# Kernel optimization log

Hardware: AMD Instinct MI355X
Metric: run time of the kernel (lower is better)

Reference implementation:

```python
import jax, jax.numpy as jnp
import numpy as np

B, T, C, H = 8, 1024, 128, 8
BLOCK = 1024  # block_size; wpe has BLOCK+1 rows, last is padding (zeros)
E = C // H


def layer_norm(x, g, b, eps=1e-5):
    mu = jnp.mean(x, axis=-1, keepdims=True)
    var = jnp.var(x, axis=-1, keepdims=True)
    return (x - mu) * jax.lax.rsqrt(var + eps) * g + b


def setup_inputs() -> dict:
    key = jax.random.key(0)
    ks = jax.random.split(key, 7)
    x = jax.random.normal(ks[0], (B, T, C), dtype=jnp.float32)
    Wq = jax.random.normal(ks[1], (C, C), dtype=jnp.float32) * 0.02
    Wk = jax.random.normal(ks[2], (C, C), dtype=jnp.float32) * 0.02
    Wv = jax.random.normal(ks[3], (C, C), dtype=jnp.float32) * 0.02
    Wp = jax.random.normal(ks[4], (C, C), dtype=jnp.float32) * 0.02
    wpe = jax.random.normal(ks[5], (BLOCK + 1, C), dtype=jnp.float32) * 0.02
    wpe = wpe.at[BLOCK].set(0.0)  # padding_idx row is zero
    ln_g = jnp.ones((C,), dtype=jnp.float32)
    ln_b = jnp.zeros((C,), dtype=jnp.float32)
    return {"x": x, "Wq": Wq, "Wk": Wk, "Wv": Wv, "Wp": Wp,
            "wpe": wpe, "ln_g": ln_g, "ln_b": ln_b}


def reference(x, Wq, Wk, Wv, Wp, wpe, ln_g, ln_b):
    Bx, Tx, Cx = x.shape
    ln_x = layer_norm(x, ln_g, ln_b)
    # project and split heads: [B, H, T, E]
    q = (ln_x @ Wq).reshape(Bx, Tx, H, E).transpose(0, 2, 1, 3)
    k = (ln_x @ Wk).reshape(Bx, Tx, H, E).transpose(0, 2, 1, 3)
    v = (ln_x @ Wv).reshape(Bx, Tx, H, E).transpose(0, 2, 1, 3)
    # relative position indices: i-j, negatives -> padding row BLOCK
    i = jnp.arange(Tx)[:, None]
    j = jnp.arange(Tx)[None, :]
    rel_idx = jnp.where(i - j < 0, BLOCK, i - j)  # [T, T]
    rel = wpe[rel_idx].reshape(Tx, Tx, H, E)      # [T, T, H, E]
    scale = 1.0 / np.sqrt(E).astype(np.float32)
    scores = (jnp.einsum('bhte,bhse->bhts', q, k)
              + jnp.einsum('tshe,bhte->bhts', rel, q)) * scale
    causal = (j <= i)  # [T, T]
    scores = jnp.where(causal[None, None, :, :], scores, jnp.float32(-jnp.inf))
    attn = jax.nn.softmax(scores, axis=-1)
    y = jnp.einsum('bhts,bhse->bhte', attn, v)    # [B, H, T, E]
    y = y.transpose(0, 2, 1, 3).reshape(Bx, Tx, Cx)
    return y @ Wp + x
```

## Files before the change

### kernel.cpp

```cpp
#include <hip/hip_runtime.h>
#include <hip/hip_bf16.h>

#define B 8
#define T 1024
#define C 128
#define H 8
#define E 16
#define BH (B*H)
#define VSTR 17

typedef __attribute__((ext_vector_type(4)))  short bf16x4;
typedef __attribute__((ext_vector_type(8)))  short bf16x8;
typedef __attribute__((ext_vector_type(16))) float f32x16;
typedef __attribute__((ext_vector_type(2)))  int   int2v;

#define QSCALE 0.36067376022224085f

__device__ __forceinline__ unsigned short bfbits(float x) {
    __hip_bfloat16 h = __float2bfloat16(x);
    return __builtin_bit_cast(unsigned short, h);
}
__device__ __forceinline__ unsigned pack2(float a, float b) {
    return (unsigned)bfbits(a) | ((unsigned)bfbits(b) << 16);
}
__device__ __forceinline__ unsigned packtr(float a, float b) {
    return (__builtin_bit_cast(unsigned, a) >> 16) | (__builtin_bit_cast(unsigned, b) & 0xffff0000u);
}

__global__ __launch_bounds__(C) void k_prep(
    const float* __restrict__ wpe,
    const float* __restrict__ Wq, const float* __restrict__ Wk,
    const float* __restrict__ Wv, const float* __restrict__ Wp,
    __hip_bfloat16* __restrict__ Wpb,
    __hip_bfloat16* __restrict__ WT,
    __hip_bfloat16* __restrict__ WpT,
    ushort* __restrict__ VT)
{
    int bid = blockIdx.x, tid = threadIdx.x;
    if (bid < 1025) {
        int h = tid >> 4, e = tid & 15;
        Wpb[((size_t)h * 1025 + bid) * 16 + e] = __float2bfloat16(wpe[(size_t)bid * C + tid]);
    } else if (bid < 1537) {
        int n = bid - 1025;
        if (n < 128)      WT[n * C + tid]          = __float2bfloat16(Wq[tid * C + n] * QSCALE);
        else if (n < 256) WT[n * C + tid]          = __float2bfloat16(Wk[tid * C + (n - 128)]);
        else if (n < 384) WT[n * C + tid]          = __float2bfloat16(Wv[tid * C + (n - 256)]);
        else              WpT[(n - 384) * C + tid] = __float2bfloat16(Wp[tid * C + (n - 384)]);
    } else {
        int bh = bid - 1537;
        ushort* row = VT + ((size_t)bh * VSTR + 16) * T + tid * 8;
        uint2 ones = make_uint2(0x3F803F80u, 0x3F803F80u);
        *(uint2*)(row)     = ones;
        *(uint2*)(row + 4) = ones;
    }
}

__global__ __launch_bounds__(256) void k_qkv(
    const float* __restrict__ x, const float* __restrict__ g, const float* __restrict__ bb,
    const __hip_bfloat16* __restrict__ WT,
    __hip_bfloat16* __restrict__ Qb, __hip_bfloat16* __restrict__ Kb,
    __hip_bfloat16* __restrict__ VT)
{
    __shared__ ushort lnlds[32 * 132];
    const int tid = threadIdx.x;
    const int mt = blockIdx.x & 255, part = blockIdx.x >> 8;

    {
        const int r = tid >> 3, qq = tid & 7;
        const float* xp = x + ((size_t)mt * 32 + r) * C + qq * 16;
        float4 x0 = ((const float4*)xp)[0];
        float4 x1 = ((const float4*)xp)[1];
        float4 x2 = ((const float4*)xp)[2];
        float4 x3 = ((const float4*)xp)[3];
        float s1v = x0.x + x0.y + x0.z + x0.w + x1.x + x1.y + x1.z + x1.w
                  + x2.x + x2.y + x2.z + x2.w + x3.x + x3.y + x3.z + x3.w;
        float s2v = x0.x*x0.x + x0.y*x0.y + x0.z*x0.z + x0.w*x0.w
                  + x1.x*x1.x + x1.y*x1.y + x1.z*x1.z + x1.w*x1.w
                  + x2.x*x2.x + x2.y*x2.y + x2.z*x2.z + x2.w*x2.w
                  + x3.x*x3.x + x3.y*x3.y + x3.z*x3.z + x3.w*x3.w;
        s1v += __shfl_xor(s1v, 1, 64); s2v += __shfl_xor(s2v, 1, 64);
        s1v += __shfl_xor(s1v, 2, 64); s2v += __shfl_xor(s2v, 2, 64);
        s1v += __shfl_xor(s1v, 4, 64); s2v += __shfl_xor(s2v, 4, 64);
        float mu  = s1v * (1.f / C);
        float var = s2v * (1.f / C) - mu * mu;
        float rs  = rsqrtf(var + 1e-5f);
        const float4* gp = (const float4*)(g  + qq * 16);
        const float4* bp = (const float4*)(bb + qq * 16);
        float4 g0 = gp[0], g1 = gp[1], g2 = gp[2], g3 = gp[3];
        float4 b0 = bp[0], b1 = bp[1], b2 = bp[2], b3 = bp[3];
        #define LNV(xx, gg, bv) (((xx) - mu) * rs * (gg) + (bv))
        uint2* dst = (uint2*)&lnlds[r * 132 + qq * 16];
        dst[0] = make_uint2(pack2(LNV(x0.x,g0.x,b0.x), LNV(x0.y,g0.y,b0.y)),
                            pack2(LNV(x0.z,g0.z,b0.z), LNV(x0.w,g0.w,b0.w)));
        dst[1] = make_uint2(pack2(LNV(x1.x,g1.x,b1.x), LNV(x1.y,g1.y,b1.y)),
                            pack2(LNV(x1.z,g1.z,b1.z), LNV(x1.w,g1.w,b1.w)));
        dst[2] = make_uint2(pack2(LNV(x2.x,g2.x,b2.x), LNV(x2.y,g2.y,b2.y)),
                            pack2(LNV(x2.z,g2.z,b2.z), LNV(x2.w,g2.w,b2.w)));
        dst[3] = make_uint2(pack2(LNV(x3.x,g3.x,b3.x), LNV(x3.y,g3.y,b3.y)),
                            pack2(LNV(x3.z,g3.z,b3.z), LNV(x3.w,g3.w,b3.w)));
        #undef LNV
    }
    __syncthreads();

    const int wv = tid >> 6, lane = tid & 63, c = lane & 31, h5 = lane >> 5;
    const int b = mt >> 5, trow = (mt & 31) * 32;
    const int nt = part * 4 + wv, n0 = nt * 32;

    bf16x8 wf[8], lf[8];
    #pragma unroll
    for (int s = 0; s < 8; ++s)
        wf[s] = *(const bf16x8*)(WT + (size_t)(n0 + c) * C + 16 * s + 8 * h5);
    #pragma unroll
    for (int s = 0; s < 8; ++s) {
        const ushort* lp = &lnlds[c * 132 + 16 * s + 8 * h5];
        bf16x4 lo = *(const bf16x4*)lp;
        bf16x4 hi = *(const bf16x4*)(lp + 4);
        lf[s] = __builtin_shufflevector(lo, hi, 0, 1, 2, 3, 4, 5, 6, 7);
    }
    f32x16 acc;
    #pragma unroll
    for (int r = 0; r < 16; ++r) acc[r] = 0.f;

    if (nt < 8) {
        #pragma unroll
        for (int s = 0; s < 8; ++s)
            acc = __builtin_amdgcn_mfma_f32_32x32x16_bf16(wf[s], lf[s], acc, 0, 0, 0);
        __hip_bfloat16* base = (nt < 4) ? Qb : Kb;
        const int nb = (nt < 4 ? n0 : n0 - 128) + 4 * h5;
        #pragma unroll
        for (int j2 = 0; j2 < 4; ++j2) {
            int n = nb + 8 * j2;
            int h = n >> 4, e = n & 15;
            uint2 w = make_uint2(pack2(acc[4*j2], acc[4*j2+1]),
                                 pack2(acc[4*j2+2], acc[4*j2+3]));
            *(uint2*)(base + ((size_t)(b * H + h) * T + trow + c) * E + e) = w;
        }
    } else {
        #pragma unroll
        for (int s = 0; s < 8; ++s)
            acc = __builtin_amdgcn_mfma_f32_32x32x16_bf16(lf[s], wf[s], acc, 0, 0, 0);
        const int ecol = n0 - 256 + c;
        const int h = ecol >> 4, e = ecol & 15;
        __hip_bfloat16* vbase = VT + ((size_t)(b * H + h) * VSTR + e) * T + trow + 4 * h5;
        #pragma unroll
        for (int j2 = 0; j2 < 4; ++j2) {
            uint2 w = make_uint2(pack2(acc[4*j2], acc[4*j2+1]),
                                 pack2(acc[4*j2+2], acc[4*j2+3]));
            *(uint2*)(vbase + 8 * j2) = w;
        }
    }
}

__global__ __launch_bounds__(256) void k_attn(
    const __hip_bfloat16* __restrict__ Qb, const __hip_bfloat16* __restrict__ Kb,
    const __hip_bfloat16* __restrict__ VT, const __hip_bfloat16* __restrict__ Wpb,
    __hip_bfloat16* __restrict__ yb)
{
    __shared__ __align__(16) float U_all[4][32 * 68];
    __shared__ float lbuf[4][32];

    const int tid = threadIdx.x, wv = tid >> 6, lane = tid & 63;
    const int h5 = lane >> 5, c = lane & 31;
    const int bh = blockIdx.x & 63;
    const int jq = 31 - (blockIdx.x >> 6);
    const int hh = bh & (H - 1);
    const int t0 = jq << 5;
    float* Uw = U_all[wv];

    const bf16x8 qf = *(const bf16x8*)(Qb + ((size_t)(bh * T + t0 + c) * E + 8 * h5));

    f32x16 Z, O;
    #pragma unroll
    for (int r = 0; r < 16; ++r) { Z[r] = 0.f; O[r] = 0.f; }

    const bool hd   = ((jq & 3) == wv);
    const int nfull = (jq > wv) ? ((jq - wv + 3) >> 2) : 0;
    const int ntl   = nfull + (hd ? 1 : 0);

    const int s0w = 32 * wv;
    const bf16x8* kp  = (const bf16x8*)(Kb  + ((size_t)(bh * T + s0w + c) * E + 8 * h5));
    const bf16x8* wph = (const bf16x8*)(Wpb + ((size_t)(hh * 1025 + t0 - s0w + c) * E + 8 * h5));
    const bf16x8* wl0 = (const bf16x8*)(Wpb + ((size_t)hh * 1025 * E + 8 * h5));
    const ushort* vap = (const ushort*)(VT + ((size_t)(bh * VSTR + c) * T + s0w + 8 * h5));

    bf16x8 kf  = *kp;
    bf16x8 wfh = *wph;
    bf16x8 wfl = (hd && ntl == 1) ? *wl0 : *(const bf16x8*)((const ushort*)wph - 32 * E);

    for (int k = 0; k < ntl; ++k) {
        const bool diag = hd && (k == ntl - 1);

        const bf16x8 va = *(const bf16x8*)vap;
        const bf16x8 vb = *(const bf16x8*)(vap + 16);

        f32x16 S   = __builtin_amdgcn_mfma_f32_32x32x16_bf16(kf,  qf, Z, 0, 0, 0);
        f32x16 Ulo = __builtin_amdgcn_mfma_f32_32x32x16_bf16(wfl, qf, Z, 0, 0, 0);
        f32x16 Uhi = __builtin_amdgcn_mfma_f32_32x32x16_bf16(wfh, qf, Z, 0, 0, 0);

        float* up = Uw + c * 68 + 4 * h5;
        *(float4*)(up +  0) = make_float4(Ulo[0],  Ulo[1],  Ulo[2],  Ulo[3]);
        *(float4*)(up +  8) = make_float4(Ulo[4],  Ulo[5],  Ulo[6],  Ulo[7]);
        *(float4*)(up + 16) = make_float4(Ulo[8],  Ulo[9],  Ulo[10], Ulo[11]);
        *(float4*)(up + 24) = make_float4(Ulo[12], Ulo[13], Ulo[14], Ulo[15]);
        *(float4*)(up + 32) = make_float4(Uhi[0],  Uhi[1],  Uhi[2],  Uhi[3]);
        *(float4*)(up + 40) = make_float4(Uhi[4],  Uhi[5],  Uhi[6],  Uhi[7]);
        *(float4*)(up + 48) = make_float4(Uhi[8],  Uhi[9],  Uhi[10], Uhi[11]);
        *(float4*)(up + 56) = make_float4(Uhi[12], Uhi[13], Uhi[14], Uhi[15]);

        kp  = (const bf16x8*)((const ushort*)kp + 128 * E);
        wph = (const bf16x8*)((const ushort*)wph - 128 * E);
        vap += 128;
        const bool diag_next = hd && (k + 1 == ntl - 1);
        const bf16x8* wlp = diag_next ? wl0 : (const bf16x8*)((const ushort*)wph - 32 * E);
        bf16x8 nkf  = *kp;
        bf16x8 nwfh = *wph;
        bf16x8 nwfl = *wlp;

        const float* ur = Uw + c * 69 + 32 - 4 * h5;
        float sc[16];
        #pragma unroll
        for (int r = 0; r < 16; ++r)
            sc[r] = S[r] + ur[-((r & 3) + 8 * (r >> 2))];
        if (diag) {
            #pragma unroll
            for (int r = 0; r < 16; ++r) {
                const int rowm = 4 * h5 + (r & 3) + 8 * (r >> 2);
                sc[r] = (rowm <= c) ? sc[r] : -1e30f;
            }
        }
        float p[16];
        #pragma unroll
        for (int r = 0; r < 16; ++r) p[r] = __builtin_amdgcn_exp2f(sc[r]);

        unsigned w0 = packtr(p[0],  p[1]),  w1 = packtr(p[2],  p[3]);
        unsigned w2 = packtr(p[4],  p[5]),  w3 = packtr(p[6],  p[7]);
        unsigned w4 = packtr(p[8],  p[9]),  w5 = packtr(p[10], p[11]);
        unsigned w6 = packtr(p[12], p[13]), w7 = packtr(p[14], p[15]);
        int2v s02 = __builtin_amdgcn_permlane32_swap((int)w0, (int)w2, false, false);
        int2v s13 = __builtin_amdgcn_permlane32_swap((int)w1, (int)w3, false, false);
        int2v s46 = __builtin_amdgcn_permlane32_swap((int)w4, (int)w6, false, false);
        int2v s57 = __builtin_amdgcn_permlane32_swap((int)w5, (int)w7, false, false);
        uint4 f1 = make_uint4((unsigned)s02.x, (unsigned)s13.x, (unsigned)s02.y, (unsigned)s13.y);
        uint4 f2 = make_uint4((unsigned)s46.x, (unsigned)s57.x, (unsigned)s46.y, (unsigned)s57.y);
        bf16x8 pb1 = __builtin_bit_cast(bf16x8, f1);
        bf16x8 pb2 = __builtin_bit_cast(bf16x8, f2);

        O = __builtin_amdgcn_mfma_f32_32x32x16_bf16(va, pb1, O, 0, 0, 0);
        O = __builtin_amdgcn_mfma_f32_32x32x16_bf16(vb, pb2, O, 0, 0, 0);

        kf = nkf; wfh = nwfh; wfl = nwfl;
    }

    __syncthreads();
    float* Of = &U_all[0][0];
    if (h5 == 0) lbuf[wv][c] = O[8];
    float* ob = Of + (wv * 32 + c) * 16;
    *(float4*)(ob + 4 * h5)     = make_float4(O[0], O[1], O[2], O[3]);
    *(float4*)(ob + 4 * h5 + 8) = make_float4(O[4], O[5], O[6], O[7]);
    __syncthreads();
    if (wv == 0) {
        float lt = lbuf[0][c] + lbuf[1][c] + lbuf[2][c] + lbuf[3][c];
        float a0=0, a1=0, a2=0, a3=0, b0=0, b1=0, b2=0, b3=0;
        #pragma unroll
        for (int w = 0; w < 4; ++w) {
            const float* op = Of + (w * 32 + c) * 16;
            float4 o1 = *(const float4*)(op + 4 * h5);
            float4 o2 = *(const float4*)(op + 4 * h5 + 8);
            a0 += o1.x; a1 += o1.y; a2 += o1.z; a3 += o1.w;
            b0 += o2.x; b1 += o2.y; b2 += o2.z; b3 += o2.w;
        }
        float inv = 1.f / lt;
        __hip_bfloat16* yp = yb + ((size_t)((bh >> 3) * T + t0 + c)) * C + (bh & 7) * E + 4 * h5;
        *(uint2*)yp       = make_uint2(pack2(a0 * inv, a1 * inv), pack2(a2 * inv, a3 * inv));
        *(uint2*)(yp + 8) = make_uint2(pack2(b0 * inv, b1 * inv), pack2(b2 * inv, b3 * inv));
    }
}

__global__ __launch_bounds__(256) void k_proj(
    const __hip_bfloat16* __restrict__ yb, const __hip_bfloat16* __restrict__ WpT,
    const float* __restrict__ x, float* __restrict__ out)
{
    __shared__ ushort ylds[32 * 132];
    const int tid = threadIdx.x;
    const size_t row0 = (size_t)blockIdx.x * 32;

    #pragma unroll
    for (int ch = 0; ch < 2; ++ch) {
        int idx = tid + ch * 256;
        int r = idx >> 4, c8 = (idx & 15) * 8;
        const ushort* src = (const ushort*)yb + (row0 + r) * C + c8;
        uint4 a = *(const uint4*)src;
        *(uint2*)&ylds[r * 132 + c8]     = make_uint2(a.x, a.y);
        *(uint2*)&ylds[r * 132 + c8 + 4] = make_uint2(a.z, a.w);
    }
    __syncthreads();

    const int wv = tid >> 6, lane = tid & 63, c = lane & 31, h5 = lane >> 5;
    const int n0 = wv * 32;
    bf16x8 wf[8], yf[8];
    #pragma unroll
    for (int s = 0; s < 8; ++s)
        wf[s] = *(const bf16x8*)(WpT + (size_t)(n0 + c) * C + 16 * s + 8 * h5);
    #pragma unroll
    for (int s = 0; s < 8; ++s) {
        const ushort* lp = &ylds[c * 132 + 16 * s + 8 * h5];
        bf16x4 lo = *(const bf16x4*)lp;
        bf16x4 hi = *(const bf16x4*)(lp + 4);
        yf[s] = __builtin_shufflevector(lo, hi, 0, 1, 2, 3, 4, 5, 6, 7);
    }
    f32x16 acc;
    #pragma unroll
    for (int r = 0; r < 16; ++r) acc[r] = 0.f;
    #pragma unroll
    for (int s = 0; s < 8; ++s)
        acc = __builtin_amdgcn_mfma_f32_32x32x16_bf16(wf[s], yf[s], acc, 0, 0, 0);

    const size_t rb = (row0 + c) * C;
    #pragma unroll
    for (int j2 = 0; j2 < 4; ++j2) {
        int n = n0 + 4 * h5 + 8 * j2;
        float4 xr = *(const float4*)(x + rb + n);
        float4 o  = make_float4(acc[4*j2] + xr.x, acc[4*j2+1] + xr.y,
                                acc[4*j2+2] + xr.z, acc[4*j2+3] + xr.w);
        *(float4*)(out + rb + n) = o;
    }
}

extern "C" void kernel_launch(void* const* d_in, const int* in_sizes, int n_in,
                              void* d_out, int out_size, void* d_ws, size_t ws_size,
                              hipStream_t stream) {
    const float* x   = (const float*)d_in[0];
    const float* Wq  = (const float*)d_in[1];
    const float* Wk  = (const float*)d_in[2];
    const float* Wv  = (const float*)d_in[3];
    const float* Wp  = (const float*)d_in[4];
    const float* wpe = (const float*)d_in[5];
    const float* g   = (const float*)d_in[6];
    const float* bb  = (const float*)d_in[7];
    float* out = (float*)d_out;

    ushort* w = (ushort*)d_ws;
    __hip_bfloat16* Qb  = (__hip_bfloat16*)(w);
    __hip_bfloat16* Kb  = (__hip_bfloat16*)(w + 1048576);
    __hip_bfloat16* VT  = (__hip_bfloat16*)(w + 2097152);
    __hip_bfloat16* Wpb = (__hip_bfloat16*)(w + 3244032);
    __hip_bfloat16* WT  = (__hip_bfloat16*)(w + 3375232);
    __hip_bfloat16* WpT = (__hip_bfloat16*)(w + 3424384);
    __hip_bfloat16* yb  = (__hip_bfloat16*)(w + 3440768);

    k_prep <<<1025 + 512 + 64, C, 0, stream>>>(wpe, Wq, Wk, Wv, Wp, Wpb, WT, WpT, (ushort*)VT);
    k_qkv  <<<768,  256, 0, stream>>>(x, g, bb, WT, Qb, Kb, VT);
    k_attn <<<2048, 256, 0, stream>>>(Qb, Kb, VT, Wpb, yb);
    k_proj <<<256,  256, 0, stream>>>(yb, WpT, x, out);
}
```

Before: 39.40 us.

## Assign contiguous key tiles per wave and reuse rel-pos MFMA across tiles

Each wave now processes a contiguous range of key tiles, walking from the diagonal backwards, instead of taking every fourth tile. Adjacent tiles share a relative-position panel, so the upper-panel MFMA result from one iteration is carried forward as the lower panel of the next. This removes one of the three score MFMAs and one Wpe load per iteration. Tile counts per wave are also balanced evenly across the four waves, at the cost of more complex index arithmetic and a tail prefetch that reads past the last tile.

```diff
diff --git a/kernel.cpp b/kernel.cpp
--- a/kernel.cpp
+++ b/kernel.cpp
@@ -173,82 +173,82 @@
     #pragma unroll
     for (int r = 0; r < 16; ++r) { Z[r] = 0.f; O[r] = 0.f; }
 
-    const bool hd   = ((jq & 3) == wv);
-    const int nfull = (jq > wv) ? ((jq - wv + 3) >> 2) : 0;
-    const int ntl   = nfull + (hd ? 1 : 0);
-
-    const int s0w = 32 * wv;
-    const bf16x8* kp  = (const bf16x8*)(Kb  + ((size_t)(bh * T + s0w + c) * E + 8 * h5));
-    const bf16x8* wph = (const bf16x8*)(Wpb + ((size_t)(hh * 1025 + t0 - s0w + c) * E + 8 * h5));
-    const bf16x8* wl0 = (const bf16x8*)(Wpb + ((size_t)hh * 1025 * E + 8 * h5));
-    const ushort* vap = (const ushort*)(VT + ((size_t)(bh * VSTR + c) * T + s0w + 8 * h5));
-
-    bf16x8 kf  = *kp;
-    bf16x8 wfh = *wph;
-    bf16x8 wfl = (hd && ntl == 1) ? *wl0 : *(const bf16x8*)((const ushort*)wph - 32 * E);
-
-    for (int k = 0; k < ntl; ++k) {
-        const bool diag = hd && (k == ntl - 1);
-
-        const bf16x8 va = *(const bf16x8*)vap;
-        const bf16x8 vb = *(const bf16x8*)(vap + 16);
-
-        f32x16 S   = __builtin_amdgcn_mfma_f32_32x32x16_bf16(kf,  qf, Z, 0, 0, 0);
-        f32x16 Ulo = __builtin_amdgcn_mfma_f32_32x32x16_bf16(wfl, qf, Z, 0, 0, 0);
-        f32x16 Uhi = __builtin_amdgcn_mfma_f32_32x32x16_bf16(wfh, qf, Z, 0, 0, 0);
-
-        float* up = Uw + c * 68 + 4 * h5;
-        *(float4*)(up +  0) = make_float4(Ulo[0],  Ulo[1],  Ulo[2],  Ulo[3]);
-        *(float4*)(up +  8) = make_float4(Ulo[4],  Ulo[5],  Ulo[6],  Ulo[7]);
-        *(float4*)(up + 16) = make_float4(Ulo[8],  Ulo[9],  Ulo[10], Ulo[11]);
-        *(float4*)(up + 24) = make_float4(Ulo[12], Ulo[13], Ulo[14], Ulo[15]);
-        *(float4*)(up + 32) = make_float4(Uhi[0],  Uhi[1],  Uhi[2],  Uhi[3]);
-        *(float4*)(up + 40) = make_float4(Uhi[4],  Uhi[5],  Uhi[6],  Uhi[7]);
-        *(float4*)(up + 48) = make_float4(Uhi[8],  Uhi[9],  Uhi[10], Uhi[11]);
-        *(float4*)(up + 56) = make_float4(Uhi[12], Uhi[13], Uhi[14], Uhi[15]);
-
-        kp  = (const bf16x8*)((const ushort*)kp + 128 * E);
-        wph = (const bf16x8*)((const ushort*)wph - 128 * E);
-        vap += 128;
-        const bool diag_next = hd && (k + 1 == ntl - 1);
-        const bf16x8* wlp = diag_next ? wl0 : (const bf16x8*)((const ushort*)wph - 32 * E);
-        bf16x8 nkf  = *kp;
-        bf16x8 nwfh = *wph;
-        bf16x8 nwfl = *wlp;
-
-        const float* ur = Uw + c * 69 + 32 - 4 * h5;
-        float sc[16];
-        #pragma unroll
-        for (int r = 0; r < 16; ++r)
-            sc[r] = S[r] + ur[-((r & 3) + 8 * (r >> 2))];
-        if (diag) {
+    const int NT = jq + 1;
+    const int qn = NT >> 2, rn = NT & 3;
+    const int off = wv * qn + (wv < rn ? wv : rn);
+    const int cnt = qn + (wv < rn ? 1 : 0);
+    const int ifirst = jq - off;
+
+    if (cnt > 0) {
+        const ushort* kp  = (const ushort*)(Kb  + ((size_t)(bh * T + 32 * ifirst + c) * E + 8 * h5));
+        const ushort* wph = (const ushort*)(Wpb + ((size_t)(hh * 1025 + 32 * off + c) * E + 8 * h5));
+        const ushort* vap = (const ushort*)(VT + ((size_t)(bh * VSTR + c) * T + 32 * ifirst + 8 * h5));
+
+        bf16x8 kf  = *(const bf16x8*)kp;
+        bf16x8 wfh = *(const bf16x8*)wph;
+        int dlo = 32 * off + c - 32; if (dlo < 0) dlo = 0;
+        const bf16x8 wfl = *(const bf16x8*)(Wpb + ((size_t)(hh * 1025 + dlo) * E + 8 * h5));
+        f32x16 Upan = __builtin_amdgcn_mfma_f32_32x32x16_bf16(wfl, qf, Z, 0, 0, 0);
+
+        for (int k = 0; k < cnt; ++k) {
+            const bool diag = (wv == 0) && (k == 0);
+
+            const bf16x8 va = *(const bf16x8*)vap;
+            const bf16x8 vb = *(const bf16x8*)(vap + 16);
+
+            f32x16 S   = __builtin_amdgcn_mfma_f32_32x32x16_bf16(kf,  qf, Z, 0, 0, 0);
+            f32x16 Uhi = __builtin_amdgcn_mfma_f32_32x32x16_bf16(wfh, qf, Z, 0, 0, 0);
+
+            float* up = Uw + c * 68 + 4 * h5;
+            *(float4*)(up +  0) = make_float4(Upan[0],  Upan[1],  Upan[2],  Upan[3]);
+            *(float4*)(up +  8) = make_float4(Upan[4],  Upan[5],  Upan[6],  Upan[7]);
+            *(float4*)(up + 16) = make_float4(Upan[8],  Upan[9],  Upan[10], Upan[11]);
+            *(float4*)(up + 24) = make_float4(Upan[12], Upan[13], Upan[14], Upan[15]);
+            *(float4*)(up + 32) = make_float4(Uhi[0],  Uhi[1],  Uhi[2],  Uhi[3]);
+            *(float4*)(up + 40) = make_float4(Uhi[4],  Uhi[5],  Uhi[6],  Uhi[7]);
+            *(float4*)(up + 48) = make_float4(Uhi[8],  Uhi[9],  Uhi[10], Uhi[11]);
+            *(float4*)(up + 56) = make_float4(Uhi[12], Uhi[13], Uhi[14], Uhi[15]);
+
+            kp  -= 32 * E;
+            wph += 32 * E;
+            vap -= 32;
+            bf16x8 nkf  = *(const bf16x8*)kp;
+            bf16x8 nwfh = *(const bf16x8*)wph;
+
+            const float* ur = Uw + c * 69 + 32 - 4 * h5;
+            float sc[16];
             #pragma unroll
-            for (int r = 0; r < 16; ++r) {
-                const int rowm = 4 * h5 + (r & 3) + 8 * (r >> 2);
-                sc[r] = (rowm <= c) ? sc[r] : -1e30f;
+            for (int r = 0; r < 16; ++r)
+                sc[r] = S[r] + ur[-((r & 3) + 8 * (r >> 2))];
+            if (diag) {
+                #pragma unroll
+                for (int r = 0; r < 16; ++r) {
+                    const int rowm = 4 * h5 + (r & 3) + 8 * (r >> 2);
+                    sc[r] = (rowm <= c) ? sc[r] : -1e30f;
+                }
             }
+            float p[16];
+            #pragma unroll
+            for (int r = 0; r < 16; ++r) p[r] = __builtin_amdgcn_exp2f(sc[r]);
+
+            unsigned w0 = packtr(p[0],  p[1]),  w1 = packtr(p[2],  p[3]);
+            unsigned w2 = packtr(p[4],  p[5]),  w3 = packtr(p[6],  p[7]);
+            unsigned w4 = packtr(p[8],  p[9]),  w5 = packtr(p[10], p[11]);
+            unsigned w6 = packtr(p[12], p[13]), w7 = packtr(p[14], p[15]);
+            int2v s02 = __builtin_amdgcn_permlane32_swap((int)w0, (int)w2, false, false);
+            int2v s13 = __builtin_amdgcn_permlane32_swap((int)w1, (int)w3, false, false);
+            int2v s46 = __builtin_amdgcn_permlane32_swap((int)w4, (int)w6, false, false);
+            int2v s57 = __builtin_amdgcn_permlane32_swap((int)w5, (int)w7, false, false);
+            uint4 f1 = make_uint4((unsigned)s02.x, (unsigned)s13.x, (unsigned)s02.y, (unsigned)s13.y);
+            uint4 f2 = make_uint4((unsigned)s46.x, (unsigned)s57.x, (unsigned)s46.y, (unsigned)s57.y);
+            bf16x8 pb1 = __builtin_bit_cast(bf16x8, f1);
+            bf16x8 pb2 = __builtin_bit_cast(bf16x8, f2);
+
+            O = __builtin_amdgcn_mfma_f32_32x32x16_bf16(va, pb1, O, 0, 0, 0);
+            O = __builtin_amdgcn_mfma_f32_32x32x16_bf16(vb, pb2, O, 0, 0, 0);
+
+            kf = nkf; wfh = nwfh; Upan = Uhi;
         }
-        float p[16];
-        #pragma unroll
-        for (int r = 0; r < 16; ++r) p[r] = __builtin_amdgcn_exp2f(sc[r]);
-
-        unsigned w0 = packtr(p[0],  p[1]),  w1 = packtr(p[2],  p[3]);
-        unsigned w2 = packtr(p[4],  p[5]),  w3 = packtr(p[6],  p[7]);
-        unsigned w4 = packtr(p[8],  p[9]),  w5 = packtr(p[10], p[11]);
-        unsigned w6 = packtr(p[12], p[13]), w7 = packtr(p[14], p[15]);
-        int2v s02 = __builtin_amdgcn_permlane32_swap((int)w0, (int)w2, false, false);
-        int2v s13 = __builtin_amdgcn_permlane32_swap((int)w1, (int)w3, false, false);
-        int2v s46 = __builtin_amdgcn_permlane32_swap((int)w4, (int)w6, false, false);
-        int2v s57 = __builtin_amdgcn_permlane32_swap((int)w5, (int)w7, false, false);
-        uint4 f1 = make_uint4((unsigned)s02.x, (unsigned)s13.x, (unsigned)s02.y, (unsigned)s13.y);
-        uint4 f2 = make_uint4((unsigned)s46.x, (unsigned)s57.x, (unsigned)s46.y, (unsigned)s57.y);
-        bf16x8 pb1 = __builtin_bit_cast(bf16x8, f1);
-        bf16x8 pb2 = __builtin_bit_cast(bf16x8, f2);
-
-        O = __builtin_amdgcn_mfma_f32_32x32x16_bf16(va, pb1, O, 0, 0, 0);
-        O = __builtin_amdgcn_mfma_f32_32x32x16_bf16(vb, pb2, O, 0, 0, 0);
-
-        kf = nkf; wfh = nwfh; wfl = nwfl;
     }
 
     __syncthreads();
```

Result: faster. 37.95 us, median of 2 (-3.7%).
